# Performance work log

Measured on AMD Instinct MI355X. Metric: run time of the kernel, lower is better.

The kernel has to match this reference:

```python
import jax, jax.numpy as jnp
import numpy as np

B, N, H, TD = 64, 100, 128, 128
EPS = 1e-5  # BatchNorm eps (torch default)


def _xavier(k, shape):
    fan_in, fan_out = shape
    lim = (6.0 / (fan_in + fan_out)) ** 0.5
    return jax.random.uniform(k, shape, jnp.float32, -lim, lim)


def setup_inputs() -> dict:
    key = jax.random.key(0)
    ks = jax.random.split(key, 12)
    inp = {}
    inp["X"] = jax.random.randint(ks[0], (B, N * N), 0, 2).astype(jnp.float32)
    inp["time"] = jax.random.uniform(ks[1], (B,), jnp.float32)
    # Time_embedding MLP: Linear(TD->H), ReLU, Linear(H->H)
    inp["Wt1"] = _xavier(ks[2], (TD, H)); inp["bt1"] = jnp.zeros((H,), jnp.float32)
    inp["Wt2"] = _xavier(ks[3], (H, H)); inp["bt2"] = jnp.zeros((H,), jnp.float32)
    # TemporalGCNBlock.time_emb: Linear(H->N) + BN(N) + ReLU
    inp["Wtn"] = _xavier(ks[4], (H, N)); inp["btn"] = jnp.zeros((N,), jnp.float32)
    inp["g_tn"] = jnp.ones((N,), jnp.float32); inp["b_tn"] = jnp.zeros((N,), jnp.float32)
    # three GCNConv layers + BN
    inp["Wg1"] = _xavier(ks[5], (2 * N, H)); inp["bg1"] = jnp.zeros((H,), jnp.float32)
    inp["g1"] = jnp.ones((H,), jnp.float32); inp["bb1"] = jnp.zeros((H,), jnp.float32)
    inp["Wg2"] = _xavier(ks[6], (H, H)); inp["bg2"] = jnp.zeros((H,), jnp.float32)
    inp["g2"] = jnp.ones((H,), jnp.float32); inp["bb2"] = jnp.zeros((H,), jnp.float32)
    inp["Wg3"] = _xavier(ks[7], (H, H)); inp["bg3"] = jnp.zeros((H,), jnp.float32)
    inp["g3"] = jnp.ones((H,), jnp.float32); inp["bb3"] = jnp.zeros((H,), jnp.float32)
    # edge head: Linear(2H->H)+BN(H), Linear(2H->1)+BN(1)
    inp["We0"] = _xavier(ks[8], (2 * H, H)); inp["be0"] = jnp.zeros((H,), jnp.float32)
    inp["g_e0"] = jnp.ones((H,), jnp.float32); inp["b_e0"] = jnp.zeros((H,), jnp.float32)
    inp["We1"] = _xavier(ks[9], (2 * H, 1)); inp["be1"] = jnp.zeros((1,), jnp.float32)
    inp["g_e1"] = jnp.ones((1,), jnp.float32); inp["b_e1"] = jnp.zeros((1,), jnp.float32)
    return inp


def _bn(x, g, b):
    # eval-mode BatchNorm with fresh running stats (mean=0, var=1)
    return g * (x / jnp.sqrt(1.0 + EPS)) + b


def _timestep_embedding(t, dim, max_positions=10000):
    half = dim // 2
    freqs = jnp.exp(jnp.arange(half, dtype=jnp.float32) * (-np.log(max_positions) / (half - 1)))
    ang = t[:, None] * freqs[None, :]  # (B, half)
    return jnp.concatenate([jnp.sin(ang), jnp.cos(ang)], axis=1)


def reference(X, time, Wt1, bt1, Wt2, bt2, Wtn, btn, g_tn, b_tn,
              Wg1, bg1, g1, bb1, Wg2, bg2, g2, bb2, Wg3, bg3, g3, bb3,
              We0, be0, g_e0, b_e0, We1, be1, g_e1, b_e1):
    eye = jnp.eye(N, dtype=jnp.float32)
    # dense_to_sparse keeps nonzeros with unit edge weight; gcn_norm adds
    # remaining self-loops then symmetric-normalizes: A_hat = D^-1/2 (A|I) D^-1/2
    A = (X.reshape(B, N, N) != 0).astype(jnp.float32)
    At = jnp.maximum(A, eye)
    dinv = At.sum(-1) ** -0.5  # deg >= 1 thanks to self-loops
    Ah = dinv[:, :, None] * At * dinv[:, None, :]  # (B,N,N)

    # global time embedding (B,H)
    temb = _timestep_embedding(time, TD)
    h = jax.nn.relu(temb @ Wt1 + bt1) @ Wt2 + bt2
    # per-node time features (B,N); repeat_interleave == same vector per node
    t_node = jax.nn.relu(_bn(h @ Wtn + btn, g_tn, b_tn))
    x = jnp.concatenate([jnp.broadcast_to(eye, (B, N, N)),
                         jnp.broadcast_to(t_node[:, None, :], (B, N, N))], axis=-1)  # (B,N,2N)

    def gcn_block(x, W, b, g, bb):
        return jax.nn.relu(_bn(jnp.einsum('bij,bjh->bih', Ah, x @ W) + b, g, bb))

    x = gcn_block(x, Wg1, bg1, g1, bb1)
    x = gcn_block(x, Wg2, bg2, g2, bb2)
    x = gcn_block(x, Wg3, bg3, g3, bb3)  # (B,N,H)

    # edge head: Linear on concat(x_i, x_j) == split projections + broadcast add
    ei = x @ We0[:H]          # (B,N,H)
    ej = x @ We0[H:]          # (B,N,H)
    e0 = ei[:, :, None, :] + ej[:, None, :, :] + be0  # (B,N,N,H)
    e0 = _bn(e0, g_e0, b_e0)
    # Linear on concat(e0, time_emb): split into edge and time projections
    s = jnp.einsum('bijh,h->bij', e0, We1[:H, 0]) + (h @ We1[H:, 0])[:, None, None] + be1[0]
    s = _bn(s, g_e1[0], b_e1[0])
    out = (s * (1.0 - eye))[..., None]  # mask diagonal, (B,N,N,1)
    return out
```

## Files before the change

### kernel.cpp

```cpp
#include <hip/hip_runtime.h>
#include <math.h>

#define NB 64
#define NN 100
#define HH 128
#define HC 16
#define NCH 8

static constexpr float EPSBN = 1e-5f;

__global__ __launch_bounds__(256) void k_setup(
    const float* __restrict__ X, const float* __restrict__ timev,
    const float* __restrict__ Wt1, const float* __restrict__ bt1,
    const float* __restrict__ Wt2, const float* __restrict__ bt2,
    const float* __restrict__ Wtn, const float* __restrict__ btn,
    const float* __restrict__ g_tn, const float* __restrict__ b_tn,
    const float* __restrict__ Wg1, const float* __restrict__ We0,
    const float* __restrict__ We1, const float* __restrict__ be1,
    const float* __restrict__ be0, const float* __restrict__ g_e0,
    const float* __restrict__ b_e0,
    float* __restrict__ Ah, float* __restrict__ rs,
    float* __restrict__ u1, float* __restrict__ Dfull,
    float* __restrict__ vi, float* __restrict__ vj) {
    __shared__ float sBuf[NN * NN];
    __shared__ float sdinv[128];
    const int bx = blockIdx.x, t = threadIdx.x;
    const float rinv = 1.0f / sqrtf(1.f + EPSBN);

    if (bx < 4 * NB) {
        const int b = bx & 63, s = bx >> 6;
        const float* Xb = X + b * NN * NN;
        float4* s4 = (float4*)sBuf;
        const float4* X4 = (const float4*)Xb;
        for (int idx = t; idx < NN * NN / 4; idx += 256) s4[idx] = X4[idx];
        __syncthreads();
        if (t < 200) {
            const int row = t >> 1, h = t & 1;
            const float4* r4 = (const float4*)(sBuf + row * NN);
            float d = 0.f;
            const int qs = h ? 13 : 0, qe = h ? 25 : 13;
            for (int q = qs; q < qe; ++q) {
                float4 v = r4[q];
                d += (v.x != 0.f ? 1.f : 0.f) + (v.y != 0.f ? 1.f : 0.f) +
                     (v.z != 0.f ? 1.f : 0.f) + (v.w != 0.f ? 1.f : 0.f);
            }
            d += __shfl_xor(d, 1);
            if (h == 0) {
                if (sBuf[row * NN + row] == 0.f) d += 1.f;
                sdinv[row] = 1.0f / sqrtf(d);
            }
        }
        __syncthreads();
        float* Ab = Ah + b * NN * NN;
        const int i0 = s * 25;
        for (int idx = t; idx < 25 * NN; idx += 256) {
            int il = idx / NN, j = idx - il * NN;
            int i = i0 + il;
            float at = (i == j) ? 1.f : (sBuf[i * NN + j] != 0.f ? 1.f : 0.f);
            Ab[i * NN + j] = sdinv[i] * at * sdinv[j];
        }
        if (t < 200) {
            const int rl = t >> 3, part = t & 7;
            const int i = i0 + rl;
            float ssum = 0.f;
            for (int j = part; j < NN; j += 8) {
                float at = (i == j) ? 1.f : (sBuf[i * NN + j] != 0.f ? 1.f : 0.f);
                ssum += at * sdinv[j];
            }
            ssum += __shfl_xor(ssum, 1, 8);
            ssum += __shfl_xor(ssum, 2, 8);
            ssum += __shfl_xor(ssum, 4, 8);
            if (part == 0) rs[b * NN + i] = sdinv[i] * ssum;
        }
        return;
    }
    if (bx < 4 * NB + NB) {
        const int b = bx - 4 * NB;
        float* s_temb = sBuf;
        float* s_h1 = sBuf + 128;
        float* s_h = sBuf + 256;
        float* s_tn = sBuf + 384;
        const float tt = timev[b];
        if (t < 128) {
            int k = t & 63;
            float f = expf((float)k * (-logf(10000.f) / 63.f));
            float a = tt * f;
            s_temb[t] = (t < 64) ? sinf(a) : cosf(a);
        }
        __syncthreads();
        if (t < 128) {
            float acc = bt1[t];
            for (int q = 0; q < HH; ++q) acc = fmaf(s_temb[q], Wt1[q * HH + t], acc);
            s_h1[t] = fmaxf(acc, 0.f);
        }
        __syncthreads();
        if (t < 128) {
            float acc = bt2[t];
            for (int q = 0; q < HH; ++q) acc = fmaf(s_h1[q], Wt2[q * HH + t], acc);
            s_h[t] = acc;
        }
        __syncthreads();
        if (t < NN) {
            float v = btn[t];
            for (int q = 0; q < HH; ++q) v = fmaf(s_h[q], Wtn[q * NN + t], v);
            s_tn[t] = fmaxf(fmaf(g_tn[t] * rinv, v, b_tn[t]), 0.f);
        }
        __syncthreads();
        if (t < 128) {
            float acc = 0.f;
            for (int n = 0; n < NN; ++n) acc = fmaf(s_tn[n], Wg1[(NN + n) * HH + t], acc);
            u1[b * HH + t] = acc;
        }
        if (t == 0) {
            float tp = 0.f;
            for (int q = 0; q < HH; ++q) tp = fmaf(s_h[q], We1[HH + q], tp);
            float K = 0.f;
            for (int hh = 0; hh < HH; ++hh)
                K += (be0[hh] * g_e0[hh] * rinv + b_e0[hh]) * We1[hh];
            Dfull[b] = tp + K + be1[0];
        }
        return;
    }
    if (t < 128) sBuf[t] = g_e0[t] * We1[t] * rinv;
    __syncthreads();
    if (t < 128) {
        float a = 0.f, cc = 0.f;
        for (int hh = 0; hh < HH; ++hh) {
            a = fmaf(We0[t * HH + hh], sBuf[hh], a);
            cc = fmaf(We0[(HH + t) * HH + hh], sBuf[hh], cc);
        }
        vi[t] = a;
        vj[t] = cc;
    }
}

__global__ __launch_bounds__(256, 2) void k_l1(
    const float* __restrict__ Ah, const float* __restrict__ Wg1,
    const float* __restrict__ u1, const float* __restrict__ rs,
    const float* __restrict__ bg1, const float* __restrict__ g1,
    const float* __restrict__ bb1, float* __restrict__ out) {
    __shared__ float sZ[112 * 20];
    const int b = blockIdx.x, hc = blockIdx.y * HC;
    const int t = threadIdx.x, jp = t & 3, ig = t >> 2;
    for (int idx = t; idx < 400; idx += 256) {
        int j = idx >> 2, c4 = idx & 3;
        *(float4*)&sZ[j * 20 + c4 * 4] = *(const float4*)&Wg1[j * HH + hc + c4 * 4];
    }
    for (int idx = t; idx < 240; idx += 256) sZ[2000 + idx] = 0.f;
    __syncthreads();
    const int r0 = ig, r1 = (ig < 36) ? 64 + ig : ig;
    float a0[16], a1[16];
#pragma unroll
    for (int c = 0; c < 16; ++c) { a0[c] = 0.f; a1[c] = 0.f; }
    const float* __restrict__ Ab = Ah + b * NN * NN;
    const int j0 = jp * 28;
#pragma unroll
    for (int s = 0; s < 7; ++s) {
        const int j = j0 + s * 4;
        float4 v0 = *(const float4*)&Ab[r0 * NN + j];
        float4 v1 = *(const float4*)&Ab[r1 * NN + j];
#pragma unroll
        for (int jj = 0; jj < 4; ++jj) {
            const float e0 = (&v0.x)[jj], e1 = (&v1.x)[jj];
            const int zr = (j + jj) * 20;
#pragma unroll
            for (int c4 = 0; c4 < 4; ++c4) {
                float4 z = *(const float4*)&sZ[zr + c4 * 4];
                a0[c4 * 4 + 0] = fmaf(e0, z.x, a0[c4 * 4 + 0]);
                a0[c4 * 4 + 1] = fmaf(e0, z.y, a0[c4 * 4 + 1]);
                a0[c4 * 4 + 2] = fmaf(e0, z.z, a0[c4 * 4 + 2]);
                a0[c4 * 4 + 3] = fmaf(e0, z.w, a0[c4 * 4 + 3]);
                a1[c4 * 4 + 0] = fmaf(e1, z.x, a1[c4 * 4 + 0]);
                a1[c4 * 4 + 1] = fmaf(e1, z.y, a1[c4 * 4 + 1]);
                a1[c4 * 4 + 2] = fmaf(e1, z.z, a1[c4 * 4 + 2]);
                a1[c4 * 4 + 3] = fmaf(e1, z.w, a1[c4 * 4 + 3]);
            }
        }
    }
#pragma unroll
    for (int c = 0; c < 16; ++c) {
        a0[c] += __shfl_xor(a0[c], 1); a0[c] += __shfl_xor(a0[c], 2);
        a1[c] += __shfl_xor(a1[c], 1); a1[c] += __shfl_xor(a1[c], 2);
    }
    if (jp == 0) {
        const float rinv = 1.0f / sqrtf(1.f + EPSBN);
        const float rs0 = rs[b * NN + r0], rs1 = rs[b * NN + r1];
        float* ob = out + b * NN * HH;
#pragma unroll
        for (int c4 = 0; c4 < 4; ++c4) {
            float4 gv = *(const float4*)&g1[hc + c4 * 4];
            float4 bbv = *(const float4*)&bb1[hc + c4 * 4];
            float4 bgv = *(const float4*)&bg1[hc + c4 * 4];
            float4 uv = *(const float4*)&u1[b * HH + hc + c4 * 4];
            float4 y0, y1;
            y0.x = fmaxf(fmaf(gv.x * rinv, a0[c4 * 4 + 0] + rs0 * uv.x + bgv.x, bbv.x), 0.f);
            y0.y = fmaxf(fmaf(gv.y * rinv, a0[c4 * 4 + 1] + rs0 * uv.y + bgv.y, bbv.y), 0.f);
            y0.z = fmaxf(fmaf(gv.z * rinv, a0[c4 * 4 + 2] + rs0 * uv.z + bgv.z, bbv.z), 0.f);
            y0.w = fmaxf(fmaf(gv.w * rinv, a0[c4 * 4 + 3] + rs0 * uv.w + bgv.w, bbv.w), 0.f);
            y1.x = fmaxf(fmaf(gv.x * rinv, a1[c4 * 4 + 0] + rs1 * uv.x + bgv.x, bbv.x), 0.f);
            y1.y = fmaxf(fmaf(gv.y * rinv, a1[c4 * 4 + 1] + rs1 * uv.y + bgv.y, bbv.y), 0.f);
            y1.z = fmaxf(fmaf(gv.z * rinv, a1[c4 * 4 + 2] + rs1 * uv.z + bgv.z, bbv.z), 0.f);
            y1.w = fmaxf(fmaf(gv.w * rinv, a1[c4 * 4 + 3] + rs1 * uv.w + bgv.w, bbv.w), 0.f);
            *(float4*)&ob[r0 * HH + hc + c4 * 4] = y0;
            if (ig < 36) *(float4*)&ob[r1 * HH + hc + c4 * 4] = y1;
        }
    }
}

template <bool LAST>
__global__ __launch_bounds__(256, 2) void k_layer(
    const float* __restrict__ Ah, const float* __restrict__ xin,
    const float* __restrict__ W, const float* __restrict__ bg,
    const float* __restrict__ g, const float* __restrict__ bb,
    const float* __restrict__ vi, const float* __restrict__ vj,
    float* __restrict__ out, float* __restrict__ psi, float* __restrict__ psj) {
    __shared__ float sW[128 * 16];
    __shared__ float sZ[112 * 20];
    const int b = blockIdx.x, hcb = blockIdx.y, hc = hcb * HC;
    const int t = threadIdx.x, jp = t & 3, ig = t >> 2;
    for (int idx = t; idx < 512; idx += 256) {
        int k = idx >> 2, c4 = idx & 3;
        int kp = ((k & 31) << 2) | (k >> 5);
        *(float4*)&sW[kp * 16 + c4 * 4] = *(const float4*)&W[k * HH + hc + c4 * 4];
    }
    for (int idx = t; idx < 240; idx += 256) sZ[2000 + idx] = 0.f;
    __syncthreads();
    const int r0 = ig, r1 = (ig < 36) ? 64 + ig : ig;
    const float* __restrict__ xb = xin + b * NN * HH;
    float a0[16], a1[16];
#pragma unroll
    for (int c = 0; c < 16; ++c) { a0[c] = 0.f; a1[c] = 0.f; }
    const int wb = jp << 4;
#pragma unroll
    for (int s = 0; s < 8; ++s) {
        const int k = (jp << 5) + s * 4;
        float4 x0 = *(const float4*)&xb[r0 * HH + k];
        float4 x1 = *(const float4*)&xb[r1 * HH + k];
#pragma unroll
        for (int kk = 0; kk < 4; ++kk) {
            const float e0 = (&x0.x)[kk], e1 = (&x1.x)[kk];
            const int wr = ((s * 4 + kk) << 6) + wb;
#pragma unroll
            for (int c4 = 0; c4 < 4; ++c4) {
                float4 w = *(const float4*)&sW[wr + c4 * 4];
                a0[c4 * 4 + 0] = fmaf(e0, w.x, a0[c4 * 4 + 0]);
                a0[c4 * 4 + 1] = fmaf(e0, w.y, a0[c4 * 4 + 1]);
                a0[c4 * 4 + 2] = fmaf(e0, w.z, a0[c4 * 4 + 2]);
                a0[c4 * 4 + 3] = fmaf(e0, w.w, a0[c4 * 4 + 3]);
                a1[c4 * 4 + 0] = fmaf(e1, w.x, a1[c4 * 4 + 0]);
                a1[c4 * 4 + 1] = fmaf(e1, w.y, a1[c4 * 4 + 1]);
                a1[c4 * 4 + 2] = fmaf(e1, w.z, a1[c4 * 4 + 2]);
                a1[c4 * 4 + 3] = fmaf(e1, w.w, a1[c4 * 4 + 3]);
            }
        }
    }
#pragma unroll
    for (int c = 0; c < 16; ++c) {
        a0[c] += __shfl_xor(a0[c], 1); a0[c] += __shfl_xor(a0[c], 2);
        a1[c] += __shfl_xor(a1[c], 1); a1[c] += __shfl_xor(a1[c], 2);
    }
    if (jp == 0) {
#pragma unroll
        for (int c4 = 0; c4 < 4; ++c4) {
            *(float4*)&sZ[r0 * 20 + c4 * 4] =
                make_float4(a0[c4 * 4 + 0], a0[c4 * 4 + 1], a0[c4 * 4 + 2], a0[c4 * 4 + 3]);
            if (ig < 36)
                *(float4*)&sZ[r1 * 20 + c4 * 4] =
                    make_float4(a1[c4 * 4 + 0], a1[c4 * 4 + 1], a1[c4 * 4 + 2], a1[c4 * 4 + 3]);
        }
    }
    __syncthreads();
#pragma unroll
    for (int c = 0; c < 16; ++c) { a0[c] = 0.f; a1[c] = 0.f; }
    const float* __restrict__ Ab = Ah + b * NN * NN;
    const int j0 = jp * 28;
#pragma unroll
    for (int s = 0; s < 7; ++s) {
        const int j = j0 + s * 4;
        float4 v0 = *(const float4*)&Ab[r0 * NN + j];
        float4 v1 = *(const float4*)&Ab[r1 * NN + j];
#pragma unroll
        for (int jj = 0; jj < 4; ++jj) {
            const float e0 = (&v0.x)[jj], e1 = (&v1.x)[jj];
            const int zr = (j + jj) * 20;
#pragma unroll
            for (int c4 = 0; c4 < 4; ++c4) {
                float4 z = *(const float4*)&sZ[zr + c4 * 4];
                a0[c4 * 4 + 0] = fmaf(e0, z.x, a0[c4 * 4 + 0]);
                a0[c4 * 4 + 1] = fmaf(e0, z.y, a0[c4 * 4 + 1]);
                a0[c4 * 4 + 2] = fmaf(e0, z.z, a0[c4 * 4 + 2]);
                a0[c4 * 4 + 3] = fmaf(e0, z.w, a0[c4 * 4 + 3]);
                a1[c4 * 4 + 0] = fmaf(e1, z.x, a1[c4 * 4 + 0]);
                a1[c4 * 4 + 1] = fmaf(e1, z.y, a1[c4 * 4 + 1]);
                a1[c4 * 4 + 2] = fmaf(e1, z.z, a1[c4 * 4 + 2]);
                a1[c4 * 4 + 3] = fmaf(e1, z.w, a1[c4 * 4 + 3]);
            }
        }
    }
#pragma unroll
    for (int c = 0; c < 16; ++c) {
        a0[c] += __shfl_xor(a0[c], 1); a0[c] += __shfl_xor(a0[c], 2);
        a1[c] += __shfl_xor(a1[c], 1); a1[c] += __shfl_xor(a1[c], 2);
    }
    if (jp == 0) {
        const float rinv = 1.0f / sqrtf(1.f + EPSBN);
        float y0[16], y1[16];
#pragma unroll
        for (int c4 = 0; c4 < 4; ++c4) {
            float4 gv = *(const float4*)&g[hc + c4 * 4];
            float4 bbv = *(const float4*)&bb[hc + c4 * 4];
            float4 bgv = *(const float4*)&bg[hc + c4 * 4];
#pragma unroll
            for (int cc = 0; cc < 4; ++cc) {
                const int c = c4 * 4 + cc;
                y0[c] = fmaxf(fmaf((&gv.x)[cc] * rinv, a0[c] + (&bgv.x)[cc], (&bbv.x)[cc]), 0.f);
                y1[c] = fmaxf(fmaf((&gv.x)[cc] * rinv, a1[c] + (&bgv.x)[cc], (&bbv.x)[cc]), 0.f);
            }
        }
        if (LAST) {
            float pi0 = 0.f, pj0 = 0.f, pi1 = 0.f, pj1 = 0.f;
#pragma unroll
            for (int c = 0; c < 16; ++c) {
                const float vic = vi[hc + c], vjc = vj[hc + c];
                pi0 = fmaf(y0[c], vic, pi0); pj0 = fmaf(y0[c], vjc, pj0);
                pi1 = fmaf(y1[c], vic, pi1); pj1 = fmaf(y1[c], vjc, pj1);
            }
            psi[(b * NN + r0) * NCH + hcb] = pi0;
            psj[(b * NN + r0) * NCH + hcb] = pj0;
            if (ig < 36) {
                psi[(b * NN + r1) * NCH + hcb] = pi1;
                psj[(b * NN + r1) * NCH + hcb] = pj1;
            }
        } else {
            float* ob = out + b * NN * HH;
#pragma unroll
            for (int c4 = 0; c4 < 4; ++c4) {
                *(float4*)&ob[r0 * HH + hc + c4 * 4] =
                    make_float4(y0[c4 * 4 + 0], y0[c4 * 4 + 1], y0[c4 * 4 + 2], y0[c4 * 4 + 3]);
                if (ig < 36)
                    *(float4*)&ob[r1 * HH + hc + c4 * 4] =
                        make_float4(y1[c4 * 4 + 0], y1[c4 * 4 + 1], y1[c4 * 4 + 2], y1[c4 * 4 + 3]);
            }
        }
    }
}

__global__ __launch_bounds__(256) void k_out(
    const float* __restrict__ psi, const float* __restrict__ psj,
    const float* __restrict__ Dfull, const float* __restrict__ g_e1,
    const float* __restrict__ b_e1, float* __restrict__ outp) {
    __shared__ float ssi[25], ssj[NN];
    const int b = blockIdx.x, i0 = blockIdx.y * 25;
    const int t = threadIdx.x;
    if (t < NN) {
        float s = 0.f;
        const float4* p = (const float4*)(psj + (b * NN + t) * NCH);
#pragma unroll
        for (int q = 0; q < NCH / 4; ++q) {
            float4 v = p[q];
            s += v.x + v.y + v.z + v.w;
        }
        ssj[t] = s;
    }
    if (t >= 128 && t < 128 + 25) {
        int i = t - 128;
        float s = 0.f;
        const float4* p = (const float4*)(psi + (b * NN + i0 + i) * NCH);
#pragma unroll
        for (int q = 0; q < NCH / 4; ++q) {
            float4 v = p[q];
            s += v.x + v.y + v.z + v.w;
        }
        ssi[i] = s;
    }
    __syncthreads();
    const float rinv = 1.0f / sqrtf(1.f + EPSBN);
    const float D = Dfull[b], ge = g_e1[0] * rinv, be = b_e1[0];
    float* ob = outp + b * NN * NN + i0 * NN;
    for (int e = t; e < 25 * NN; e += 256) {
        int ii = e / NN, j = e - ii * NN;
        float v = fmaf(ge, ssi[ii] + ssj[j] + D, be);
        ob[e] = (i0 + ii == j) ? 0.f : v;
    }
}

extern "C" void kernel_launch(void* const* d_in, const int* in_sizes, int n_in,
                              void* d_out, int out_size, void* d_ws, size_t ws_size,
                              hipStream_t stream) {
    const float* X    = (const float*)d_in[0];
    const float* timev= (const float*)d_in[1];
    const float* Wt1  = (const float*)d_in[2];
    const float* bt1  = (const float*)d_in[3];
    const float* Wt2  = (const float*)d_in[4];
    const float* bt2  = (const float*)d_in[5];
    const float* Wtn  = (const float*)d_in[6];
    const float* btn  = (const float*)d_in[7];
    const float* g_tn = (const float*)d_in[8];
    const float* b_tn = (const float*)d_in[9];
    const float* Wg1  = (const float*)d_in[10];
    const float* bg1  = (const float*)d_in[11];
    const float* g1   = (const float*)d_in[12];
    const float* bb1  = (const float*)d_in[13];
    const float* Wg2  = (const float*)d_in[14];
    const float* bg2  = (const float*)d_in[15];
    const float* g2   = (const float*)d_in[16];
    const float* bb2  = (const float*)d_in[17];
    const float* Wg3  = (const float*)d_in[18];
    const float* bg3  = (const float*)d_in[19];
    const float* g3   = (const float*)d_in[20];
    const float* bb3  = (const float*)d_in[21];
    const float* We0  = (const float*)d_in[22];
    const float* be0  = (const float*)d_in[23];
    const float* g_e0 = (const float*)d_in[24];
    const float* b_e0 = (const float*)d_in[25];
    const float* We1  = (const float*)d_in[26];
    const float* be1  = (const float*)d_in[27];
    const float* g_e1 = (const float*)d_in[28];
    const float* b_e1 = (const float*)d_in[29];

    float* ws = (float*)d_ws;
    float* Ah    = ws;
    float* rs    = Ah + 640000;
    float* u1    = rs + 6400;
    float* Dfull = u1 + 8192;
    float* vi    = Dfull + 64;
    float* vj    = vi + 128;
    float* x1    = vj + 128;
    float* x2    = x1 + 819200;
    float* psi   = x1;
    float* psj   = x1 + 51200;

    k_setup<<<dim3(4 * NB + NB + 1), dim3(256), 0, stream>>>(
        X, timev, Wt1, bt1, Wt2, bt2, Wtn, btn, g_tn, b_tn, Wg1, We0, We1, be1,
        be0, g_e0, b_e0, Ah, rs, u1, Dfull, vi, vj);

    k_l1<<<dim3(NB, NCH), dim3(256), 0, stream>>>(Ah, Wg1, u1, rs, bg1, g1, bb1, x1);
    k_layer<false><<<dim3(NB, NCH), dim3(256), 0, stream>>>(Ah, x1, Wg2, bg2, g2, bb2,
                                                            nullptr, nullptr, x2,
                                                            nullptr, nullptr);
    k_layer<true><<<dim3(NB, NCH), dim3(256), 0, stream>>>(Ah, x2, Wg3, bg3, g3, bb3,
                                                           vi, vj, nullptr, psi, psj);

    k_out<<<dim3(NB, 4), dim3(256), 0, stream>>>(psi, psj, Dfull, g_e1, b_e1,
                                                 (float*)d_out);
}
```

Measured before the change: 54.86 us.

## Fuse adjacency setup, time MLP and first GCN layer into one per-batch kernel

```diff
diff --git a/kernel.cpp b/kernel.cpp
--- a/kernel.cpp
+++ b/kernel.cpp
@@ -9,77 +9,86 @@
 
 static constexpr float EPSBN = 1e-5f;
 
-__global__ __launch_bounds__(256) void k_setup(
+__global__ __launch_bounds__(256) void k_init(
     const float* __restrict__ X, const float* __restrict__ timev,
     const float* __restrict__ Wt1, const float* __restrict__ bt1,
     const float* __restrict__ Wt2, const float* __restrict__ bt2,
     const float* __restrict__ Wtn, const float* __restrict__ btn,
     const float* __restrict__ g_tn, const float* __restrict__ b_tn,
-    const float* __restrict__ Wg1, const float* __restrict__ We0,
-    const float* __restrict__ We1, const float* __restrict__ be1,
-    const float* __restrict__ be0, const float* __restrict__ g_e0,
-    const float* __restrict__ b_e0,
-    float* __restrict__ Ah, float* __restrict__ rs,
-    float* __restrict__ u1, float* __restrict__ Dfull,
-    float* __restrict__ vi, float* __restrict__ vj) {
-    __shared__ float sBuf[NN * NN];
-    __shared__ float sdinv[128];
+    const float* __restrict__ Wg1, const float* __restrict__ bg1,
+    const float* __restrict__ g1, const float* __restrict__ bb1,
+    const float* __restrict__ We0, const float* __restrict__ We1,
+    const float* __restrict__ be1, const float* __restrict__ be0,
+    const float* __restrict__ g_e0, const float* __restrict__ b_e0,
+    float* __restrict__ Ah, float* __restrict__ Dfull,
+    float* __restrict__ vi, float* __restrict__ vj, float* __restrict__ x1) {
+    __shared__ float sBuf[10000];
+    __shared__ float sdinv[104];
+    __shared__ float srs[104];
+    __shared__ float su1[128];
+    __shared__ float sml[512];
     const int bx = blockIdx.x, t = threadIdx.x;
     const float rinv = 1.0f / sqrtf(1.f + EPSBN);
 
-    if (bx < 4 * NB) {
-        const int b = bx & 63, s = bx >> 6;
-        const float* Xb = X + b * NN * NN;
+    if (bx == NB) {
+        if (t < 128) sml[t] = g_e0[t] * We1[t] * rinv;
+        __syncthreads();
+        if (t < 128) {
+            float a = 0.f, cc = 0.f;
+            for (int hh = 0; hh < HH; ++hh) {
+                a = fmaf(We0[t * HH + hh], sml[hh], a);
+                cc = fmaf(We0[(HH + t) * HH + hh], sml[hh], cc);
+            }
+            vi[t] = a;
+            vj[t] = cc;
+        }
+        return;
+    }
+    const int b = bx;
+    {
         float4* s4 = (float4*)sBuf;
-        const float4* X4 = (const float4*)Xb;
+        const float4* X4 = (const float4*)(X + b * NN * NN);
         for (int idx = t; idx < NN * NN / 4; idx += 256) s4[idx] = X4[idx];
-        __syncthreads();
-        if (t < 200) {
-            const int row = t >> 1, h = t & 1;
-            const float4* r4 = (const float4*)(sBuf + row * NN);
-            float d = 0.f;
-            const int qs = h ? 13 : 0, qe = h ? 25 : 13;
-            for (int q = qs; q < qe; ++q) {
-                float4 v = r4[q];
-                d += (v.x != 0.f ? 1.f : 0.f) + (v.y != 0.f ? 1.f : 0.f) +
-                     (v.z != 0.f ? 1.f : 0.f) + (v.w != 0.f ? 1.f : 0.f);
-            }
-            d += __shfl_xor(d, 1);
-            if (h == 0) {
-                if (sBuf[row * NN + row] == 0.f) d += 1.f;
-                sdinv[row] = 1.0f / sqrtf(d);
-            }
-        }
-        __syncthreads();
-        float* Ab = Ah + b * NN * NN;
-        const int i0 = s * 25;
-        for (int idx = t; idx < 25 * NN; idx += 256) {
-            int il = idx / NN, j = idx - il * NN;
-            int i = i0 + il;
-            float at = (i == j) ? 1.f : (sBuf[i * NN + j] != 0.f ? 1.f : 0.f);
-            Ab[i * NN + j] = sdinv[i] * at * sdinv[j];
-        }
-        if (t < 200) {
-            const int rl = t >> 3, part = t & 7;
-            const int i = i0 + rl;
-            float ssum = 0.f;
-            for (int j = part; j < NN; j += 8) {
-                float at = (i == j) ? 1.f : (sBuf[i * NN + j] != 0.f ? 1.f : 0.f);
-                ssum += at * sdinv[j];
-            }
-            ssum += __shfl_xor(ssum, 1, 8);
-            ssum += __shfl_xor(ssum, 2, 8);
-            ssum += __shfl_xor(ssum, 4, 8);
-            if (part == 0) rs[b * NN + i] = sdinv[i] * ssum;
-        }
-        return;
-    }
-    if (bx < 4 * NB + NB) {
-        const int b = bx - 4 * NB;
-        float* s_temb = sBuf;
-        float* s_h1 = sBuf + 128;
-        float* s_h = sBuf + 256;
-        float* s_tn = sBuf + 384;
+    }
+    __syncthreads();
+    if (t < 200) {
+        const int row = t >> 1, h = t & 1;
+        const float4* r4 = (const float4*)(sBuf + row * NN);
+        float d = 0.f;
+        const int qs = h ? 13 : 0, qe = h ? 25 : 13;
+        for (int q = qs; q < qe; ++q) {
+            float4 v = r4[q];
+            d += (v.x != 0.f ? 1.f : 0.f) + (v.y != 0.f ? 1.f : 0.f) +
+                 (v.z != 0.f ? 1.f : 0.f) + (v.w != 0.f ? 1.f : 0.f);
+        }
+        d += __shfl_xor(d, 1);
+        if (h == 0) {
+            if (sBuf[row * NN + row] == 0.f) d += 1.f;
+            sdinv[row] = 1.0f / sqrtf(d);
+        }
+    }
+    __syncthreads();
+    float* Ab = Ah + b * NN * NN;
+    for (int idx = t; idx < NN * NN; idx += 256) {
+        int i = idx / NN, j = idx - i * NN;
+        float at = (i == j) ? 1.f : (sBuf[idx] != 0.f ? 1.f : 0.f);
+        Ab[idx] = sdinv[i] * at * sdinv[j];
+    }
+    if (t < 200) {
+        const int row = t >> 1, h = t & 1;
+        float ssum = 0.f;
+        for (int j = h; j < NN; j += 2) {
+            float at = (row == j) ? 1.f : (sBuf[row * NN + j] != 0.f ? 1.f : 0.f);
+            ssum += at * sdinv[j];
+        }
+        ssum += __shfl_xor(ssum, 1);
+        if (h == 0) srs[row] = sdinv[row] * ssum;
+    }
+    {
+        float* s_temb = sml;
+        float* s_h1 = sml + 128;
+        float* s_h = sml + 256;
+        float* s_tn = sml + 384;
         const float tt = timev[b];
         if (t < 128) {
             int k = t & 63;
@@ -109,7 +118,7 @@
         if (t < 128) {
             float acc = 0.f;
             for (int n = 0; n < NN; ++n) acc = fmaf(s_tn[n], Wg1[(NN + n) * HH + t], acc);
-            u1[b * HH + t] = acc;
+            su1[t] = acc;
         }
         if (t == 0) {
             float tp = 0.f;
@@ -119,90 +128,74 @@
                 K += (be0[hh] * g_e0[hh] * rinv + b_e0[hh]) * We1[hh];
             Dfull[b] = tp + K + be1[0];
         }
-        return;
-    }
-    if (t < 128) sBuf[t] = g_e0[t] * We1[t] * rinv;
-    __syncthreads();
-    if (t < 128) {
-        float a = 0.f, cc = 0.f;
-        for (int hh = 0; hh < HH; ++hh) {
-            a = fmaf(We0[t * HH + hh], sBuf[hh], a);
-            cc = fmaf(We0[(HH + t) * HH + hh], sBuf[hh], cc);
-        }
-        vi[t] = a;
-        vj[t] = cc;
-    }
-}
-
-__global__ __launch_bounds__(256, 2) void k_l1(
-    const float* __restrict__ Ah, const float* __restrict__ Wg1,
-    const float* __restrict__ u1, const float* __restrict__ rs,
-    const float* __restrict__ bg1, const float* __restrict__ g1,
-    const float* __restrict__ bb1, float* __restrict__ out) {
-    __shared__ float sZ[112 * 20];
-    const int b = blockIdx.x, hc = blockIdx.y * HC;
-    const int t = threadIdx.x, jp = t & 3, ig = t >> 2;
-    for (int idx = t; idx < 400; idx += 256) {
-        int j = idx >> 2, c4 = idx & 3;
-        *(float4*)&sZ[j * 20 + c4 * 4] = *(const float4*)&Wg1[j * HH + hc + c4 * 4];
-    }
-    for (int idx = t; idx < 240; idx += 256) sZ[2000 + idx] = 0.f;
-    __syncthreads();
+    }
+    const int jp = t & 3, ig = t >> 2;
     const int r0 = ig, r1 = (ig < 36) ? 64 + ig : ig;
-    float a0[16], a1[16];
-#pragma unroll
-    for (int c = 0; c < 16; ++c) { a0[c] = 0.f; a1[c] = 0.f; }
-    const float* __restrict__ Ab = Ah + b * NN * NN;
-    const int j0 = jp * 28;
-#pragma unroll
-    for (int s = 0; s < 7; ++s) {
-        const int j = j0 + s * 4;
-        float4 v0 = *(const float4*)&Ab[r0 * NN + j];
-        float4 v1 = *(const float4*)&Ab[r1 * NN + j];
-#pragma unroll
-        for (int jj = 0; jj < 4; ++jj) {
-            const float e0 = (&v0.x)[jj], e1 = (&v1.x)[jj];
-            const int zr = (j + jj) * 20;
+    float* sZ = sBuf;
+    float* ob = x1 + b * NN * HH;
+    for (int hcb = 0; hcb < 8; ++hcb) {
+        const int hc = hcb * HC;
+        __syncthreads();
+        for (int idx = t; idx < 400; idx += 256) {
+            int j = idx >> 2, c4 = idx & 3;
+            *(float4*)&sZ[j * 20 + c4 * 4] = *(const float4*)&Wg1[j * HH + hc + c4 * 4];
+        }
+        for (int idx = t; idx < 240; idx += 256) sZ[2000 + idx] = 0.f;
+        __syncthreads();
+        float a0[16], a1[16];
+#pragma unroll
+        for (int c = 0; c < 16; ++c) { a0[c] = 0.f; a1[c] = 0.f; }
+        const int j0 = jp * 28;
+#pragma unroll
+        for (int s = 0; s < 7; ++s) {
+            const int j = j0 + s * 4;
+            float4 v0 = *(const float4*)&Ab[r0 * NN + j];
+            float4 v1 = *(const float4*)&Ab[r1 * NN + j];
+#pragma unroll
+            for (int jj = 0; jj < 4; ++jj) {
+                const float e0 = (&v0.x)[jj], e1 = (&v1.x)[jj];
+                const int zr = (j + jj) * 20;
+#pragma unroll
+                for (int c4 = 0; c4 < 4; ++c4) {
+                    float4 z = *(const float4*)&sZ[zr + c4 * 4];
+                    a0[c4 * 4 + 0] = fmaf(e0, z.x, a0[c4 * 4 + 0]);
+                    a0[c4 * 4 + 1] = fmaf(e0, z.y, a0[c4 * 4 + 1]);
+                    a0[c4 * 4 + 2] = fmaf(e0, z.z, a0[c4 * 4 + 2]);
+                    a0[c4 * 4 + 3] = fmaf(e0, z.w, a0[c4 * 4 + 3]);
+                    a1[c4 * 4 + 0] = fmaf(e1, z.x, a1[c4 * 4 + 0]);
+                    a1[c4 * 4 + 1] = fmaf(e1, z.y, a1[c4 * 4 + 1]);
+                    a1[c4 * 4 + 2] = fmaf(e1, z.z, a1[c4 * 4 + 2]);
+                    a1[c4 * 4 + 3] = fmaf(e1, z.w, a1[c4 * 4 + 3]);
+                }
+            }
+        }
+#pragma unroll
+        for (int c = 0; c < 16; ++c) {
+            a0[c] += __shfl_xor(a0[c], 1); a0[c] += __shfl_xor(a0[c], 2);
+            a1[c] += __shfl_xor(a1[c], 1); a1[c] += __shfl_xor(a1[c], 2);
+        }
+        if (jp == 0) {
+            const float rs0 = srs[r0], rs1 = srs[r1];
 #pragma unroll
             for (int c4 = 0; c4 < 4; ++c4) {
-                float4 z = *(const float4*)&sZ[zr + c4 * 4];
-                a0[c4 * 4 + 0] = fmaf(e0, z.x, a0[c4 * 4 + 0]);
-                a0[c4 * 4 + 1] = fmaf(e0, z.y, a0[c4 * 4 + 1]);
-                a0[c4 * 4 + 2] = fmaf(e0, z.z, a0[c4 * 4 + 2]);
-                a0[c4 * 4 + 3] = fmaf(e0, z.w, a0[c4 * 4 + 3]);
-                a1[c4 * 4 + 0] = fmaf(e1, z.x, a1[c4 * 4 + 0]);
-                a1[c4 * 4 + 1] = fmaf(e1, z.y, a1[c4 * 4 + 1]);
-                a1[c4 * 4 + 2] = fmaf(e1, z.z, a1[c4 * 4 + 2]);
-                a1[c4 * 4 + 3] = fmaf(e1, z.w, a1[c4 * 4 + 3]);
-            }
-        }
-    }
-#pragma unroll
-    for (int c = 0; c < 16; ++c) {
-        a0[c] += __shfl_xor(a0[c], 1); a0[c] += __shfl_xor(a0[c], 2);
-        a1[c] += __shfl_xor(a1[c], 1); a1[c] += __shfl_xor(a1[c], 2);
-    }
-    if (jp == 0) {
-        const float rinv = 1.0f / sqrtf(1.f + EPSBN);
-        const float rs0 = rs[b * NN + r0], rs1 = rs[b * NN + r1];
-        float* ob = out + b * NN * HH;
-#pragma unroll
-        for (int c4 = 0; c4 < 4; ++c4) {
-            float4 gv = *(const float4*)&g1[hc + c4 * 4];
-            float4 bbv = *(const float4*)&bb1[hc + c4 * 4];
-            float4 bgv = *(const float4*)&bg1[hc + c4 * 4];
-            float4 uv = *(const float4*)&u1[b * HH + hc + c4 * 4];
-            float4 y0, y1;
-            y0.x = fmaxf(fmaf(gv.x * rinv, a0[c4 * 4 + 0] + rs0 * uv.x + bgv.x, bbv.x), 0.f);
-            y0.y = fmaxf(fmaf(gv.y * rinv, a0[c4 * 4 + 1] + rs0 * uv.y + bgv.y, bbv.y), 0.f);
-            y0.z = fmaxf(fmaf(gv.z * rinv, a0[c4 * 4 + 2] + rs0 * uv.z + bgv.z, bbv.z), 0.f);
-            y0.w = fmaxf(fmaf(gv.w * rinv, a0[c4 * 4 + 3] + rs0 * uv.w + bgv.w, bbv.w), 0.f);
-            y1.x = fmaxf(fmaf(gv.x * rinv, a1[c4 * 4 + 0] + rs1 * uv.x + bgv.x, bbv.x), 0.f);
-            y1.y = fmaxf(fmaf(gv.y * rinv, a1[c4 * 4 + 1] + rs1 * uv.y + bgv.y, bbv.y), 0.f);
-            y1.z = fmaxf(fmaf(gv.z * rinv, a1[c4 * 4 + 2] + rs1 * uv.z + bgv.z, bbv.z), 0.f);
-            y1.w = fmaxf(fmaf(gv.w * rinv, a1[c4 * 4 + 3] + rs1 * uv.w + bgv.w, bbv.w), 0.f);
-            *(float4*)&ob[r0 * HH + hc + c4 * 4] = y0;
-            if (ig < 36) *(float4*)&ob[r1 * HH + hc + c4 * 4] = y1;
+                float4 gv = *(const float4*)&g1[hc + c4 * 4];
+                float4 bbv = *(const float4*)&bb1[hc + c4 * 4];
+                float4 bgv = *(const float4*)&bg1[hc + c4 * 4];
+                float4 uv = *(const float4*)&su1[hc + c4 * 4];
+                float4 y0, y1;
+#pragma unroll
+                for (int cc = 0; cc < 4; ++cc) {
+                    const int c = c4 * 4 + cc;
+                    (&y0.x)[cc] = fmaxf(fmaf((&gv.x)[cc] * rinv,
+                                             a0[c] + rs0 * (&uv.x)[cc] + (&bgv.x)[cc],
+                                             (&bbv.x)[cc]), 0.f);
+                    (&y1.x)[cc] = fmaxf(fmaf((&gv.x)[cc] * rinv,
+                                             a1[c] + rs1 * (&uv.x)[cc] + (&bgv.x)[cc],
+                                             (&bbv.x)[cc]), 0.f);
+                }
+                *(float4*)&ob[r0 * HH + hc + c4 * 4] = y0;
+                if (ig < 36) *(float4*)&ob[r1 * HH + hc + c4 * 4] = y1;
+            }
         }
     }
 }
@@ -420,9 +413,7 @@
 
     float* ws = (float*)d_ws;
     float* Ah    = ws;
-    float* rs    = Ah + 640000;
-    float* u1    = rs + 6400;
-    float* Dfull = u1 + 8192;
+    float* Dfull = Ah + 640000;
     float* vi    = Dfull + 64;
     float* vj    = vi + 128;
     float* x1    = vj + 128;
@@ -430,11 +421,11 @@
     float* psi   = x1;
     float* psj   = x1 + 51200;
 
-    k_setup<<<dim3(4 * NB + NB + 1), dim3(256), 0, stream>>>(
-        X, timev, Wt1, bt1, Wt2, bt2, Wtn, btn, g_tn, b_tn, Wg1, We0, We1, be1,
-        be0, g_e0, b_e0, Ah, rs, u1, Dfull, vi, vj);
-
-    k_l1<<<dim3(NB, NCH), dim3(256), 0, stream>>>(Ah, Wg1, u1, rs, bg1, g1, bb1, x1);
+    k_init<<<dim3(NB + 1), dim3(256), 0, stream>>>(
+        X, timev, Wt1, bt1, Wt2, bt2, Wtn, btn, g_tn, b_tn,
+        Wg1, bg1, g1, bb1, We0, We1, be1, be0, g_e0, b_e0,
+        Ah, Dfull, vi, vj, x1);
+
     k_layer<false><<<dim3(NB, NCH), dim3(256), 0, stream>>>(Ah, x1, Wg2, bg2, g2, bb2,
                                                             nullptr, nullptr, x2,
                                                             nullptr, nullptr);
```

Result: slower. 93.57 us (+70.6%).
